# Optimization experiments

Hardware: AMD Instinct MI355X
Metric: run time of the kernel (lower is better)

Reference implementation:

```python
import jax, jax.numpy as jnp
import numpy as np

EPS = 1e-5  # torch BatchNorm1d default

def _batchnorm(h, g, b):
    # training-mode BN over batch axis, biased variance (matches torch)
    mu = h.mean(axis=0)
    var = ((h - mu) ** 2).mean(axis=0)
    return g * (h - mu) / jnp.sqrt(var + EPS) + b


def setup_inputs() -> dict:
    key = jax.random.key(0)
    ks = jax.random.split(key, 8)
    B = 65536
    x = jax.random.normal(ks[0], (B, 784), dtype=jnp.float32)
    W0 = jax.random.normal(ks[1], (10, 784), dtype=jnp.float32) * (1.0 / np.sqrt(784))
    b0 = jax.random.normal(ks[2], (10,), dtype=jnp.float32) * 0.01
    g0 = jnp.ones((10,), dtype=jnp.float32)
    beta0 = jnp.zeros((10,), dtype=jnp.float32)
    Ws = jax.random.normal(ks[3], (62, 10, 10), dtype=jnp.float32) * (1.0 / np.sqrt(10))
    bs = jax.random.normal(ks[4], (62, 10), dtype=jnp.float32) * 0.01
    gs = jnp.ones((62, 10), dtype=jnp.float32)
    betas = jnp.zeros((62, 10), dtype=jnp.float32)
    Wf = jax.random.normal(ks[5], (10, 10), dtype=jnp.float32) * (1.0 / np.sqrt(10))
    bf = jax.random.normal(ks[6], (10,), dtype=jnp.float32) * 0.01
    return {"x": x, "W0": W0, "b0": b0, "g0": g0, "beta0": beta0,
            "Ws": Ws, "bs": bs, "gs": gs, "betas": betas, "Wf": Wf, "bf": bf}


def reference(x, W0, b0, g0, beta0, Ws, bs, gs, betas, Wf, bf):
    # Linear(784->10) + BN
    h = x @ W0.T + b0                     # [B,10]
    h = _batchnorm(h, g0, beta0)
    def step(h, layer):
        W, b, g, beta = layer
        h = h @ W.T + b
        h = _batchnorm(h, g, beta)
        return h, None
    h, _ = jax.lax.scan(step, h, (Ws, bs, gs, betas))
    # final Linear(10,10), no BN
    return h @ Wf.T + bf
```

## Files before the change

kernel.cpp:

```cpp
#include <hip/hip_runtime.h>

#define NROWS 65536
#define DIN   784
#define NF    10
#define NL    62
#define NSTAT 65
#define NB    1024
#define ROWS_PB 64
#define KCH   196
#define TPW   7

#define STATSF_OFF_B 0
#define PART_OFF_B   512

#define KEEP4(v4) asm volatile("" : "+v"(v4.x), "+v"(v4.y), "+v"(v4.z), "+v"(v4.w))

__global__ __launch_bounds__(256, 2) void passA(const float* __restrict__ x,
                                                const float* __restrict__ W0,
                                                const float* __restrict__ b0,
                                                float* __restrict__ zout,
                                                float* __restrict__ partials) {
  __shared__ float xs[4 * 64 * 30];
  const int tid = threadIdx.x;
  const int lane = tid & 63;
  const int wv = __builtin_amdgcn_readfirstlane(tid >> 6);
  const int rowbase = blockIdx.x * ROWS_PB;

  const float* xw = x + (size_t)rowbase * DIN + wv * KCH;
  const float* wp = W0 + wv * KCH;
  float* xsw = xs + wv * (64 * 30);

  int goff[TPW], soff[TPW];
#pragma unroll
  for (int q = 0; q < TPW; ++q) {
    int g = lane + q * 64;
    int row = g / 7, pos = g % 7;
    goff[q] = row * DIN + pos * 4;
    soff[q] = row * 30 + pos * 4;
  }

  float acc[NF];
#pragma unroll
  for (int j = 0; j < NF; ++j) acc[j] = (wv == 0) ? b0[j] : 0.f;

  float4 Aq[TPW], Bq[TPW];
#pragma unroll
  for (int q = 0; q < TPW; ++q) Aq[q] = *(const float4*)(xw + goff[q]);
#pragma unroll
  for (int q = 0; q < TPW; ++q) {
    float2* d = (float2*)(xsw + soff[q]);
    d[0] = make_float2(Aq[q].x, Aq[q].y);
    d[1] = make_float2(Aq[q].z, Aq[q].w);
  }

#define STEP(bi, NXT, DOLOAD)                                                  \
  do {                                                                         \
    if (DOLOAD) {                                                              \
      _Pragma("unroll") for (int q = 0; q < TPW; ++q)                          \
          NXT[q] = *(const float4*)(xw + ((bi) + 1) * 28 + goff[q]);           \
    }                                                                          \
    float xv[28];                                                              \
    _Pragma("unroll") for (int i = 0; i < 28; i += 2) {                        \
      float2 v = *(const float2*)(xsw + lane * 30 + i);                        \
      xv[i] = v.x; xv[i + 1] = v.y;                                            \
    }                                                                          \
    _Pragma("unroll") for (int e = 0; e < 28; ++e) {                           \
      _Pragma("unroll") for (int j = 0; j < NF; ++j)                           \
          acc[j] = fmaf(xv[e], wp[j * DIN + (bi)*28 + e], acc[j]);             \
    }                                                                          \
    if (DOLOAD) {                                                              \
      _Pragma("unroll") for (int q = 0; q < TPW; ++q) KEEP4(NXT[q]);           \
      _Pragma("unroll") for (int q = 0; q < TPW; ++q) {                        \
        float2* d = (float2*)(xsw + soff[q]);                                  \
        d[0] = make_float2(NXT[q].x, NXT[q].y);                                \
        d[1] = make_float2(NXT[q].z, NXT[q].w);                                \
      }                                                                        \
    }                                                                          \
  } while (0)

  STEP(0, Bq, 1); STEP(1, Aq, 1); STEP(2, Bq, 1);
  STEP(3, Aq, 1); STEP(4, Bq, 1); STEP(5, Aq, 1);
  STEP(6, Bq, 0);
#undef STEP

  __syncthreads();
  float (*comb)[NF] = (float(*)[NF])xs;
#pragma unroll
  for (int j = 0; j < NF; ++j) comb[wv * 64 + lane][j] = acc[j];
  __syncthreads();
  float a[NF];
#pragma unroll
  for (int j = 0; j < NF; ++j)
    a[j] = comb[0 * 64 + lane][j] + comb[1 * 64 + lane][j] +
           comb[2 * 64 + lane][j] + comb[3 * 64 + lane][j];

  if (wv == 0) {
    float* zr = zout + (size_t)(rowbase + lane) * NF;
#pragma unroll
    for (int j = 0; j < NF; j += 2) *(float2*)(zr + j) = make_float2(a[j], a[j + 1]);
  }

  float vals[NSTAT];
  {
    int v = 0;
#pragma unroll
    for (int j = 0; j < NF; ++j) vals[v++] = a[j];
#pragma unroll
    for (int i = 0; i < NF; ++i)
#pragma unroll
      for (int j = i; j < NF; ++j) vals[v++] = a[i] * a[j];
  }
  const int kb2 = wv * 17, ke2 = (wv == 3) ? NSTAT : wv * 17 + 17;
#pragma unroll
  for (int k = 0; k < NSTAT; ++k) {
    if (k >= kb2 && k < ke2) {
      float s = vals[k];
#pragma unroll
      for (int m = 1; m < 64; m <<= 1) s += __shfl_xor(s, m, 64);
      if (lane == 0) partials[k * NB + blockIdx.x] = s;
    }
  }
}

__global__ __launch_bounds__(128, 1) void passB(const float* __restrict__ partials,
                                                const float* __restrict__ Ws,
                                                const float* __restrict__ g0,
                                                const float* __restrict__ gs,
                                                const float* __restrict__ betas,
                                                const float* __restrict__ Wfin,
                                                const float* __restrict__ bfin,
                                                float* __restrict__ statsf) {
  __shared__ float WL[NL * 100];
  __shared__ float gsl[NL * NF];
  __shared__ double Sd[NSTAT];
  __shared__ float tb[NF * NF];
  __shared__ float svl[2 * NF];
  const int tid = threadIdx.x;
  const int lane = tid & 63;
  const int wv = __builtin_amdgcn_readfirstlane(tid >> 6);
  const int il = lane < NF ? lane : NF - 1;
  const bool owner = lane < NF;

  for (int i = tid; i < NL * 100; i += 128) WL[i] = Ws[i];
  for (int i = tid; i < NL * NF; i += 128) gsl[i] = gs[i];

  {
    const int k0 = (wv == 0) ? 0 : 33, k1 = (wv == 0) ? 33 : NSTAT;
    for (int k = k0; k < k1; ++k) {
      const float* pr = partials + (size_t)k * NB;
      double s = 0.0;
#pragma unroll
      for (int i = 0; i < NB / 64; ++i) s += (double)pr[i * 64 + lane];
#pragma unroll
      for (int m = 1; m < 64; m <<= 1) s += __shfl_xor(s, m, 64);
      if (lane == 0) Sd[k] = s;
    }
  }
  __syncthreads();

  const double invN = 1.0 / (double)NROWS;
  float s_own = 0.f;
  if (wv == 0) {
    const int idxd = NF + il * NF - (il * (il - 1)) / 2;
    double mu_own = Sd[il] * invN;
    double var_own = Sd[idxd] * invN - mu_own * mu_own;
    double s0d = (double)g0[il] / sqrt(var_own + 1e-5);
    s_own = (float)s0d;
    if (owner) svl[il] = s_own;
  }
  __syncthreads();
  float sj0[NF];
#pragma unroll
  for (int j = 0; j < NF; ++j) sj0[j] = svl[j];

  float CovR[NF];
  float Mrow[NF], dvv[NF];
  if (wv == 0) {
    double mu_own = Sd[il] * invN;
#pragma unroll
    for (int j = 0; j < NF; ++j) {
      int a_ = il < j ? il : j, b_ = il < j ? j : il;
      int idx = NF + a_ * NF - (a_ * (a_ - 1)) / 2 + (b_ - a_);
      double cov = Sd[idx] * invN - mu_own * (Sd[j] * invN);
      CovR[j] = ((float)cov * s_own) * sj0[j];
    }
  } else {
#pragma unroll
    for (int j = 0; j < NF; ++j) {
      Mrow[j] = (il == j) ? sj0[j] : 0.f;
      dvv[j] = -(float)(Sd[j] * invN) * sj0[j];
    }
  }

  float CzR[NF], Pt[NF], Dt[NF], s2 = 0.f;
  for (int k = 0; k < NL; ++k) {
    const float* W = &WL[k * 100];
    if (wv == 0) {
      float VR[NF];
#pragma unroll
      for (int l = 0; l < NF; ++l) {
        float t = 0.f;
#pragma unroll
        for (int m = 0; m < NF; ++m) t = fmaf(CovR[m], W[l * 10 + m], t);
        VR[l] = t;
      }
      if (owner) {
        float2* d = (float2*)(tb + il * NF);
#pragma unroll
        for (int h = 0; h < 5; ++h) d[h] = make_float2(VR[2 * h], VR[2 * h + 1]);
      }
      float YR[NF];
#pragma unroll
      for (int l = 0; l < NF; ++l) YR[l] = tb[l * NF + il];
#pragma unroll
      for (int j = 0; j < NF; ++j) {
        float t = 0.f;
#pragma unroll
        for (int l = 0; l < NF; ++l) t = fmaf(YR[l], W[j * 10 + l], t);
        CzR[j] = t;
      }
      float cz_own = CzR[0];
#pragma unroll
      for (int j = 1; j < NF; ++j) cz_own = (il == j) ? CzR[j] : cz_own;
      s2 = gsl[k * NF + il] / sqrtf(cz_own + 1e-5f);
      if (owner) svl[((k + 1) & 1) * NF + il] = s2;
    } else {
#pragma unroll
      for (int j = 0; j < NF; ++j) {
        float t = 0.f, u = 0.f;
#pragma unroll
        for (int l = 0; l < NF; ++l) {
          t = fmaf(Mrow[l], W[j * 10 + l], t);
          u = fmaf(dvv[l], W[j * 10 + l], u);
        }
        Pt[j] = t; Dt[j] = u;
      }
    }
    __syncthreads();
    float sjn[NF];
#pragma unroll
    for (int j = 0; j < NF; ++j) sjn[j] = svl[((k + 1) & 1) * NF + j];
    if (wv == 0) {
#pragma unroll
      for (int j = 0; j < NF; ++j) CovR[j] = CzR[j] * s2 * sjn[j];
    } else {
#pragma unroll
      for (int j = 0; j < NF; ++j) { Mrow[j] = Pt[j] * sjn[j]; dvv[j] = Dt[j] * sjn[j]; }
    }
  }

  if (wv == 1) {
    float cvecf[NF];
#pragma unroll
    for (int j = 0; j < NF; ++j) cvecf[j] = dvv[j] + betas[(NL - 1) * NF + j];
    float Ff[NF], cf[NF];
#pragma unroll
    for (int j = 0; j < NF; ++j) {
      float t = 0.f, u = bfin[j];
#pragma unroll
      for (int l = 0; l < NF; ++l) {
        t = fmaf(Mrow[l], Wfin[j * 10 + l], t);
        u = fmaf(cvecf[l], Wfin[j * 10 + l], u);
      }
      Ff[j] = t; cf[j] = u;
    }
    if (owner) {
#pragma unroll
      for (int j = 0; j < NF; ++j) statsf[il * NF + j] = Ff[j];
    }
    if (lane == 0) {
#pragma unroll
      for (int j = 0; j < NF; ++j) statsf[100 + j] = cf[j];
    }
  }
}

__global__ __launch_bounds__(256) void passC(float* __restrict__ z_inout,
                                             const float* __restrict__ statsf) {
  const int r = blockIdx.x * 256 + threadIdx.x;
  float* pz = z_inout + (size_t)r * NF;
  float zr[NF];
#pragma unroll
  for (int j = 0; j < NF; j += 2) {
    float2 v = *(const float2*)(pz + j);
    zr[j] = v.x; zr[j + 1] = v.y;
  }
  float acc2[NF];
#pragma unroll
  for (int j = 0; j < NF; ++j) acc2[j] = statsf[100 + j];
#pragma unroll
  for (int l = 0; l < NF; ++l)
#pragma unroll
    for (int j = 0; j < NF; ++j) acc2[j] = fmaf(zr[l], statsf[l * 10 + j], acc2[j]);
#pragma unroll
  for (int j = 0; j < NF; j += 2) *(float2*)(pz + j) = make_float2(acc2[j], acc2[j + 1]);
}

extern "C" void kernel_launch(void* const* d_in, const int* in_sizes, int n_in,
                              void* d_out, int out_size, void* d_ws, size_t ws_size,
                              hipStream_t stream) {
  const float* x     = (const float*)d_in[0];
  const float* W0    = (const float*)d_in[1];
  const float* b0    = (const float*)d_in[2];
  const float* g0    = (const float*)d_in[3];
  const float* Ws    = (const float*)d_in[5];
  const float* gs    = (const float*)d_in[7];
  const float* betas = (const float*)d_in[8];
  const float* Wfin  = (const float*)d_in[9];
  const float* bfin  = (const float*)d_in[10];
  float* out = (float*)d_out;

  float* statsf   = (float*)((char*)d_ws + STATSF_OFF_B);
  float* partials = (float*)((char*)d_ws + PART_OFF_B);

  passA<<<NB, 256, 0, stream>>>(x, W0, b0, out, partials);
  passB<<<1, 128, 0, stream>>>(partials, Ws, g0, gs, betas, Wfin, bfin, statsf);
  passC<<<256, 256, 0, stream>>>(out, statsf);
}
```

Baseline: 421.5 us.

## Rewrite GEMV pass with single-wave direct global-to-LDS double buffering; fp64 covariance recursion

The first pass now runs one 64-thread wave per block covering the full 784-wide K dimension. The x tiles are streamed with global_load_lds directly into a swizzled, double-buffered LDS tile, which drops the four-wave split and the cross-wave combine. The statistics reduction now uses all 65 shuffle reductions in the single wave. The covariance recursion in passB is also moved to double precision for accuracy. The cost is far fewer threads per block (1024 blocks of 64 threads), which may lower the memory-level parallelism available to a bandwidth-bound 200 MB read, plus slower fp64 math in the serial passB.

```diff
diff --git a/kernel.cpp b/kernel.cpp
--- a/kernel.cpp
+++ b/kernel.cpp
@@ -6,120 +6,106 @@
 #define NL    62
 #define NSTAT 65
 #define NB    1024
-#define ROWS_PB 64
-#define KCH   196
-#define TPW   7
+#define NT    49
 
 #define STATSF_OFF_B 0
 #define PART_OFF_B   512
 
-#define KEEP4(v4) asm volatile("" : "+v"(v4.x), "+v"(v4.y), "+v"(v4.z), "+v"(v4.w))
-
-__global__ __launch_bounds__(256, 2) void passA(const float* __restrict__ x,
-                                                const float* __restrict__ W0,
-                                                const float* __restrict__ b0,
-                                                float* __restrict__ zout,
-                                                float* __restrict__ partials) {
-  __shared__ float xs[4 * 64 * 30];
-  const int tid = threadIdx.x;
-  const int lane = tid & 63;
-  const int wv = __builtin_amdgcn_readfirstlane(tid >> 6);
-  const int rowbase = blockIdx.x * ROWS_PB;
-
-  const float* xw = x + (size_t)rowbase * DIN + wv * KCH;
-  const float* wp = W0 + wv * KCH;
-  float* xsw = xs + wv * (64 * 30);
-
-  int goff[TPW], soff[TPW];
-#pragma unroll
-  for (int q = 0; q < TPW; ++q) {
-    int g = lane + q * 64;
-    int row = g / 7, pos = g % 7;
-    goff[q] = row * DIN + pos * 4;
-    soff[q] = row * 30 + pos * 4;
-  }
+__device__ __forceinline__ void gload_lds16(const float* g, float* l) {
+  __builtin_amdgcn_global_load_lds(
+      (const __attribute__((address_space(1))) void*)g,
+      (__attribute__((address_space(3))) void*)l, 16, 0, 0);
+}
+
+__global__ __launch_bounds__(64, 4) void passA(const float* __restrict__ x,
+                                               const float* __restrict__ W0,
+                                               const float* __restrict__ b0,
+                                               float* __restrict__ zout,
+                                               float* __restrict__ partials) {
+  __shared__ __align__(16) float xs[2][1024];
+  const int lane = threadIdx.x;
+  const int rowbase = blockIdx.x * 64;
+  const float* xb = x + (size_t)rowbase * DIN;
+
+  const int srow = lane >> 2;
+  const int scol = ((lane & 3) ^ ((lane >> 3) & 3)) << 2;
+  const size_t sidx = (size_t)srow * DIN + scol;
+
+#define STAGE(t, b)                                                            \
+  do {                                                                         \
+    asm volatile("s_waitcnt lgkmcnt(0)" ::: "memory");  \
+    const float* s_ = xb + (size_t)(t) * 16 + sidx;                            \
+    gload_lds16(s_ + 0 * 16 * DIN, &xs[b][0 * 256]);                           \
+    gload_lds16(s_ + 1 * 16 * DIN, &xs[b][1 * 256]);                           \
+    gload_lds16(s_ + 2 * 16 * DIN, &xs[b][2 * 256]);                           \
+    gload_lds16(s_ + 3 * 16 * DIN, &xs[b][3 * 256]);                           \
+  } while (0)
 
   float acc[NF];
 #pragma unroll
-  for (int j = 0; j < NF; ++j) acc[j] = (wv == 0) ? b0[j] : 0.f;
-
-  float4 Aq[TPW], Bq[TPW];
-#pragma unroll
-  for (int q = 0; q < TPW; ++q) Aq[q] = *(const float4*)(xw + goff[q]);
-#pragma unroll
-  for (int q = 0; q < TPW; ++q) {
-    float2* d = (float2*)(xsw + soff[q]);
-    d[0] = make_float2(Aq[q].x, Aq[q].y);
-    d[1] = make_float2(Aq[q].z, Aq[q].w);
-  }
-
-#define STEP(bi, NXT, DOLOAD)                                                  \
+  for (int j = 0; j < NF; ++j) acc[j] = b0[j];
+
+  const int rbase = lane << 4;
+  const int rx = (lane >> 1) & 3;
+
+#define COMP(t, b)                                                             \
   do {                                                                         \
-    if (DOLOAD) {                                                              \
-      _Pragma("unroll") for (int q = 0; q < TPW; ++q)                          \
-          NXT[q] = *(const float4*)(xw + ((bi) + 1) * 28 + goff[q]);           \
-    }                                                                          \
-    float xv[28];                                                              \
-    _Pragma("unroll") for (int i = 0; i < 28; i += 2) {                        \
-      float2 v = *(const float2*)(xsw + lane * 30 + i);                        \
-      xv[i] = v.x; xv[i + 1] = v.y;                                            \
-    }                                                                          \
-    _Pragma("unroll") for (int e = 0; e < 28; ++e) {                           \
-      _Pragma("unroll") for (int j = 0; j < NF; ++j)                           \
-          acc[j] = fmaf(xv[e], wp[j * DIN + (bi)*28 + e], acc[j]);             \
-    }                                                                          \
-    if (DOLOAD) {                                                              \
-      _Pragma("unroll") for (int q = 0; q < TPW; ++q) KEEP4(NXT[q]);           \
-      _Pragma("unroll") for (int q = 0; q < TPW; ++q) {                        \
-        float2* d = (float2*)(xsw + soff[q]);                                  \
-        d[0] = make_float2(NXT[q].x, NXT[q].y);                                \
-        d[1] = make_float2(NXT[q].z, NXT[q].w);                                \
+    _Pragma("unroll") for (int i = 0; i < 4; ++i) {                            \
+      float4 v = *(const float4*)(&xs[b][rbase + (((i) ^ rx) << 2)]);          \
+      const float* wk = W0 + (t) * 16 + (i << 2);       \
+      _Pragma("unroll") for (int j = 0; j < NF; ++j) {                         \
+        acc[j] = fmaf(v.x, wk[j * DIN + 0], acc[j]);                           \
+        acc[j] = fmaf(v.y, wk[j * DIN + 1], acc[j]);                           \
+        acc[j] = fmaf(v.z, wk[j * DIN + 2], acc[j]);                           \
+        acc[j] = fmaf(v.w, wk[j * DIN + 3], acc[j]);                           \
       }                                                                        \
     }                                                                          \
   } while (0)
 
-  STEP(0, Bq, 1); STEP(1, Aq, 1); STEP(2, Bq, 1);
-  STEP(3, Aq, 1); STEP(4, Bq, 1); STEP(5, Aq, 1);
-  STEP(6, Bq, 0);
-#undef STEP
-
-  __syncthreads();
-  float (*comb)[NF] = (float(*)[NF])xs;
-#pragma unroll
-  for (int j = 0; j < NF; ++j) comb[wv * 64 + lane][j] = acc[j];
-  __syncthreads();
-  float a[NF];
-#pragma unroll
-  for (int j = 0; j < NF; ++j)
-    a[j] = comb[0 * 64 + lane][j] + comb[1 * 64 + lane][j] +
-           comb[2 * 64 + lane][j] + comb[3 * 64 + lane][j];
-
-  if (wv == 0) {
+  STAGE(0, 0);
+  for (int t = 0; t < NT - 1; ++t) {
+    STAGE(t + 1, (t + 1) & 1);
+    asm volatile("s_waitcnt vmcnt(4)" ::: "memory");
+    __builtin_amdgcn_sched_barrier(0);
+    COMP(t, t & 1);
+  }
+  asm volatile("s_waitcnt vmcnt(0)" ::: "memory");
+  __builtin_amdgcn_sched_barrier(0);
+  COMP(NT - 1, 0);
+#undef STAGE
+#undef COMP
+
+  {
     float* zr = zout + (size_t)(rowbase + lane) * NF;
 #pragma unroll
-    for (int j = 0; j < NF; j += 2) *(float2*)(zr + j) = make_float2(a[j], a[j + 1]);
-  }
-
-  float vals[NSTAT];
+    for (int j = 0; j < NF; j += 2) *(float2*)(zr + j) = make_float2(acc[j], acc[j + 1]);
+  }
+
+#define RED(s)                                                                 \
+  do {                                                                         \
+    _Pragma("unroll") for (int m_ = 1; m_ < 64; m_ <<= 1) s += __shfl_xor(s, m_, 64); \
+  } while (0)
   {
-    int v = 0;
-#pragma unroll
-    for (int j = 0; j < NF; ++j) vals[v++] = a[j];
-#pragma unroll
-    for (int i = 0; i < NF; ++i)
-#pragma unroll
-      for (int j = i; j < NF; ++j) vals[v++] = a[i] * a[j];
-  }
-  const int kb2 = wv * 17, ke2 = (wv == 3) ? NSTAT : wv * 17 + 17;
-#pragma unroll
-  for (int k = 0; k < NSTAT; ++k) {
-    if (k >= kb2 && k < ke2) {
-      float s = vals[k];
-#pragma unroll
-      for (int m = 1; m < 64; m <<= 1) s += __shfl_xor(s, m, 64);
-      if (lane == 0) partials[k * NB + blockIdx.x] = s;
-    }
-  }
+    int kk = 0;
+#pragma unroll
+    for (int i = 0; i < NF; ++i) {
+      float s = acc[i];
+      RED(s);
+      if (lane == (kk & 63)) partials[kk * NB + blockIdx.x] = s;
+      ++kk;
+    }
+#pragma unroll
+    for (int i = 0; i < NF; ++i) {
+#pragma unroll
+      for (int j = i; j < NF; ++j) {
+        float s = acc[i] * acc[j];
+        RED(s);
+        if (lane == (kk & 63)) partials[kk * NB + blockIdx.x] = s;
+        ++kk;
+      }
+    }
+  }
+#undef RED
 }
 
 __global__ __launch_bounds__(128, 1) void passB(const float* __restrict__ partials,
@@ -130,18 +116,22 @@
                                                 const float* __restrict__ Wfin,
                                                 const float* __restrict__ bfin,
                                                 float* __restrict__ statsf) {
-  __shared__ float WL[NL * 100];
-  __shared__ float gsl[NL * NF];
+  __shared__ double WLd[NL * 100];
+  __shared__ float  WL[NL * 100];
+  __shared__ float  gsl[NL * NF];
   __shared__ double Sd[NSTAT];
-  __shared__ float tb[NF * NF];
-  __shared__ float svl[2 * NF];
+  __shared__ double tbd[NF * NF];
+  __shared__ double svld[2 * NF];
+  __shared__ float  svl[2 * NF];
   const int tid = threadIdx.x;
   const int lane = tid & 63;
   const int wv = __builtin_amdgcn_readfirstlane(tid >> 6);
   const int il = lane < NF ? lane : NF - 1;
   const bool owner = lane < NF;
 
-  for (int i = tid; i < NL * 100; i += 128) WL[i] = Ws[i];
+  for (int i = tid; i < NL * 100; i += 128) {
+    float w = Ws[i]; WL[i] = w; WLd[i] = (double)w;
+  }
   for (int i = tid; i < NL * NF; i += 128) gsl[i] = gs[i];
 
   {
@@ -159,72 +149,71 @@
   __syncthreads();
 
   const double invN = 1.0 / (double)NROWS;
-  float s_own = 0.f;
   if (wv == 0) {
     const int idxd = NF + il * NF - (il * (il - 1)) / 2;
     double mu_own = Sd[il] * invN;
     double var_own = Sd[idxd] * invN - mu_own * mu_own;
-    double s0d = (double)g0[il] / sqrt(var_own + 1e-5);
-    s_own = (float)s0d;
-    if (owner) svl[il] = s_own;
+    double s0 = (double)g0[il] / sqrt(var_own + 1e-5);
+    if (owner) { svld[il] = s0; svl[il] = (float)s0; }
   }
   __syncthreads();
-  float sj0[NF];
-#pragma unroll
-  for (int j = 0; j < NF; ++j) sj0[j] = svl[j];
-
-  float CovR[NF];
+
+  double CovRd[NF];
   float Mrow[NF], dvv[NF];
   if (wv == 0) {
+    double s_own = svld[il];
     double mu_own = Sd[il] * invN;
 #pragma unroll
     for (int j = 0; j < NF; ++j) {
       int a_ = il < j ? il : j, b_ = il < j ? j : il;
       int idx = NF + a_ * NF - (a_ * (a_ - 1)) / 2 + (b_ - a_);
       double cov = Sd[idx] * invN - mu_own * (Sd[j] * invN);
-      CovR[j] = ((float)cov * s_own) * sj0[j];
+      CovRd[j] = cov * s_own * svld[j];
     }
   } else {
 #pragma unroll
     for (int j = 0; j < NF; ++j) {
-      Mrow[j] = (il == j) ? sj0[j] : 0.f;
-      dvv[j] = -(float)(Sd[j] * invN) * sj0[j];
-    }
-  }
-
-  float CzR[NF], Pt[NF], Dt[NF], s2 = 0.f;
+      float sj = svl[j];
+      Mrow[j] = (il == j) ? sj : 0.f;
+      dvv[j] = -(float)(Sd[j] * invN) * sj;
+    }
+  }
+
+  double CzRd[NF];
+  float Pt[NF], Dt[NF], s2f = 0.f;
   for (int k = 0; k < NL; ++k) {
-    const float* W = &WL[k * 100];
+    const int slot = ((k + 1) & 1) * NF;
     if (wv == 0) {
-      float VR[NF];
+      const double* Wd = &WLd[k * 100];
+      double VR[NF];
 #pragma unroll
       for (int l = 0; l < NF; ++l) {
-        float t = 0.f;
-#pragma unroll
-        for (int m = 0; m < NF; ++m) t = fmaf(CovR[m], W[l * 10 + m], t);
+        double t = 0.0;
+#pragma unroll
+        for (int m = 0; m < NF; ++m) t = fma(CovRd[m], Wd[l * 10 + m], t);
         VR[l] = t;
       }
       if (owner) {
-        float2* d = (float2*)(tb + il * NF);
-#pragma unroll
-        for (int h = 0; h < 5; ++h) d[h] = make_float2(VR[2 * h], VR[2 * h + 1]);
-      }
-      float YR[NF];
-#pragma unroll
-      for (int l = 0; l < NF; ++l) YR[l] = tb[l * NF + il];
+#pragma unroll
+        for (int l = 0; l < NF; ++l) tbd[il * NF + l] = VR[l];
+      }
+      double YR[NF];
+#pragma unroll
+      for (int l = 0; l < NF; ++l) YR[l] = tbd[l * NF + il];
 #pragma unroll
       for (int j = 0; j < NF; ++j) {
-        float t = 0.f;
-#pragma unroll
-        for (int l = 0; l < NF; ++l) t = fmaf(YR[l], W[j * 10 + l], t);
-        CzR[j] = t;
-      }
-      float cz_own = CzR[0];
-#pragma unroll
-      for (int j = 1; j < NF; ++j) cz_own = (il == j) ? CzR[j] : cz_own;
-      s2 = gsl[k * NF + il] / sqrtf(cz_own + 1e-5f);
-      if (owner) svl[((k + 1) & 1) * NF + il] = s2;
+        double t = 0.0;
+#pragma unroll
+        for (int l = 0; l < NF; ++l) t = fma(YR[l], Wd[j * 10 + l], t);
+        CzRd[j] = t;
+      }
+      double cz_own = CzRd[0];
+#pragma unroll
+      for (int j = 1; j < NF; ++j) cz_own = (il == j) ? CzRd[j] : cz_own;
+      s2f = gsl[k * NF + il] / sqrtf((float)cz_own + 1e-5f);
+      if (owner) { svld[slot + il] = (double)s2f; svl[slot + il] = s2f; }
     } else {
+      const float* W = &WL[k * 100];
 #pragma unroll
       for (int j = 0; j < NF; ++j) {
         float t = 0.f, u = 0.f;
@@ -237,15 +226,16 @@
       }
     }
     __syncthreads();
-    float sjn[NF];
-#pragma unroll
-    for (int j = 0; j < NF; ++j) sjn[j] = svl[((k + 1) & 1) * NF + j];
     if (wv == 0) {
-#pragma unroll
-      for (int j = 0; j < NF; ++j) CovR[j] = CzR[j] * s2 * sjn[j];
+      double s2d = (double)s2f;
+#pragma unroll
+      for (int j = 0; j < NF; ++j) CovRd[j] = CzRd[j] * s2d * svld[slot + j];
     } else {
 #pragma unroll
-      for (int j = 0; j < NF; ++j) { Mrow[j] = Pt[j] * sjn[j]; dvv[j] = Dt[j] * sjn[j]; }
+      for (int j = 0; j < NF; ++j) {
+        float sj = svl[slot + j];
+        Mrow[j] = Pt[j] * sj; dvv[j] = Dt[j] * sj;
+      }
     }
   }
 
@@ -313,7 +303,7 @@
   float* statsf   = (float*)((char*)d_ws + STATSF_OFF_B);
   float* partials = (float*)((char*)d_ws + PART_OFF_B);
 
-  passA<<<NB, 256, 0, stream>>>(x, W0, b0, out, partials);
+  passA<<<NB, 64, 0, stream>>>(x, W0, b0, out, partials);
   passB<<<1, 128, 0, stream>>>(partials, Ws, g0, gs, betas, Wfin, bfin, statsf);
   passC<<<256, 256, 0, stream>>>(out, statsf);
 }
```

Result: slower. 523.1 us (+24.1%).
